# Optimization experiments

Measured on AMD Instinct MI355X. Metric: run time of the kernel, lower is better.

The kernel has to match this reference:

```python
import jax, jax.numpy as jnp
import numpy as np

B, SQ, SK, H, NH = 4, 512, 2048, 1024, 16
HD = H // NH
LN_EPS = 1e-12
NEG_INF = float('-inf')


def setup_inputs() -> dict:
    key = jax.random.key(0)
    ks = jax.random.split(key, 6)
    hidden_states = jax.random.normal(ks[0], (B, SQ, H), dtype=jnp.float32)
    encoder_hidden_states = jax.random.normal(ks[1], (B, SK, H), dtype=jnp.float32)
    mask = jax.random.randint(ks[2], (B, SK), 0, 2).astype(jnp.int32)
    mask = mask.at[:, 0].set(1)  # guarantee >=1 valid key per row (avoid all -inf softmax)
    scale = 1.0 / np.sqrt(H)
    q_w = jax.random.normal(ks[3], (H, H), dtype=jnp.float32) * scale
    k_w = jax.random.normal(ks[4], (H, H), dtype=jnp.float32) * scale
    return {
        'hidden_states': hidden_states,
        'encoder_hidden_states': encoder_hidden_states,
        'encoder_attention_mask': mask,
        'q_w': q_w,
        'q_b': jnp.zeros((H,), jnp.float32),
        'k_w': k_w,
        'k_b': jnp.zeros((H,), jnp.float32),
        'ln_g': jnp.ones((H,), jnp.float32),
        'ln_b': jnp.zeros((H,), jnp.float32),
    }


def _layernorm(x, g, b):
    mu = jnp.mean(x, axis=-1, keepdims=True)
    var = jnp.mean(jnp.square(x - mu), axis=-1, keepdims=True)
    return (x - mu) * jax.lax.rsqrt(var + LN_EPS) * g + b


def reference(hidden_states, encoder_hidden_states, encoder_attention_mask,
              q_w, q_b, k_w, k_b, ln_g, ln_b):
    bsz, sq, _ = hidden_states.shape
    hs = _layernorm(hidden_states, ln_g, ln_b)
    # torch Linear: y = x @ W.T + b
    q = (hs @ q_w.T + q_b).reshape(bsz, sq, NH, HD).transpose(0, 2, 1, 3)      # b h q d
    k = (encoder_hidden_states @ k_w.T + k_b).reshape(bsz, -1, NH, HD).transpose(0, 2, 1, 3)  # b h k d
    v = encoder_hidden_states.reshape(bsz, -1, NH, HD).transpose(0, 2, 1, 3)   # b h k d (no v projection)
    scores = jnp.einsum('bhqd,bhkd->bhqk', q, k) / np.sqrt(HD)
    scores = jnp.where(encoder_attention_mask[:, None, None, :] == 0, NEG_INF, scores)
    probs = jax.nn.softmax(scores, axis=-1)
    ctx = jnp.einsum('bhqk,bhkd->bhqd', probs, v)
    ctx = ctx.transpose(0, 2, 1, 3).reshape(bsz, sq, H)
    return ctx, scores
```

## Files before the change

kernel.cpp:

```cpp
#include <hip/hip_runtime.h>
#include <math.h>

#define H 1024
#define NH 16
#define HD 64
#define B_ 4
#define SQ 512
#define SK 2048
#define MASKED_SCORE -1e30f

typedef unsigned short ushort_t;
typedef __attribute__((ext_vector_type(8))) short short8_t;
typedef __attribute__((ext_vector_type(4))) float f32x4;
typedef __attribute__((ext_vector_type(4))) unsigned short us4;

__device__ inline ushort_t bf_hi(float x) { return (ushort_t)(__float_as_uint(x) >> 16); }
__device__ inline ushort_t bf_lo(float x) {
    float hf = __uint_as_float(__float_as_uint(x) & 0xffff0000u);
    return (ushort_t)(__float_as_uint(x - hf) >> 16);
}

__global__ __launch_bounds__(256) void ln_split_kernel(const float* __restrict__ x,
                                                       const float* __restrict__ g,
                                                       const float* __restrict__ bb,
                                                       ushort_t* __restrict__ hi,
                                                       ushort_t* __restrict__ lo) {
    const int row = blockIdx.x;
    const int tid = threadIdx.x;
    const float4 v = *(const float4*)&x[(size_t)row * H + tid * 4];
    float s  = v.x + v.y + v.z + v.w;
    float ss = v.x * v.x + v.y * v.y + v.z * v.z + v.w * v.w;
    #pragma unroll
    for (int o = 32; o > 0; o >>= 1) { s += __shfl_down(s, o); ss += __shfl_down(ss, o); }
    __shared__ float red_s[4], red_ss[4];
    const int wv = tid >> 6, ln = tid & 63;
    if (ln == 0) { red_s[wv] = s; red_ss[wv] = ss; }
    __syncthreads();
    s  = red_s[0] + red_s[1] + red_s[2] + red_s[3];
    ss = red_ss[0] + red_ss[1] + red_ss[2] + red_ss[3];
    const float mu   = s * (1.0f / H);
    const float var  = ss * (1.0f / H) - mu * mu;
    const float rstd = rsqrtf(var + 1e-12f);
    const float4 gv = *(const float4*)&g[tid * 4];
    const float4 bv = *(const float4*)&bb[tid * 4];
    float o0 = (v.x - mu) * rstd * gv.x + bv.x;
    float o1 = (v.y - mu) * rstd * gv.y + bv.y;
    float o2 = (v.z - mu) * rstd * gv.z + bv.z;
    float o3 = (v.w - mu) * rstd * gv.w + bv.w;
    us4 h4, l4;
    h4.x = bf_hi(o0); h4.y = bf_hi(o1); h4.z = bf_hi(o2); h4.w = bf_hi(o3);
    l4.x = bf_lo(o0); l4.y = bf_lo(o1); l4.z = bf_lo(o2); l4.w = bf_lo(o3);
    *(us4*)&hi[(size_t)row * H + tid * 4] = h4;
    *(us4*)&lo[(size_t)row * H + tid * 4] = l4;
}

__global__ __launch_bounds__(256) void ehs_split_tr(const float* __restrict__ ehs,
                                                    ushort_t* __restrict__ eh, ushort_t* __restrict__ el,
                                                    ushort_t* __restrict__ vh, ushort_t* __restrict__ vl) {
    __shared__ float Tf[64][68];
    const int tid = threadIdx.x;
    const int k0 = blockIdx.x * 64;
    const int h = blockIdx.y, b = blockIdx.z;
    const int r = tid >> 2, c0 = (tid & 3) << 4;
    const size_t gidx = (size_t)(b * SK + k0 + r) * H + h * HD + c0;
    float fv[16];
    #pragma unroll
    for (int j = 0; j < 4; ++j) {
        const float4 v = *(const float4*)&ehs[gidx + 4 * j];
        fv[4 * j + 0] = v.x; fv[4 * j + 1] = v.y; fv[4 * j + 2] = v.z; fv[4 * j + 3] = v.w;
        Tf[r][c0 + 4 * j + 0] = v.x; Tf[r][c0 + 4 * j + 1] = v.y;
        Tf[r][c0 + 4 * j + 2] = v.z; Tf[r][c0 + 4 * j + 3] = v.w;
    }
    short8_t H0, H1, L0, L1;
    #pragma unroll
    for (int j = 0; j < 8; ++j) {
        H0[j] = (short)bf_hi(fv[j]);     H1[j] = (short)bf_hi(fv[8 + j]);
        L0[j] = (short)bf_lo(fv[j]);     L1[j] = (short)bf_lo(fv[8 + j]);
    }
    *(short8_t*)&eh[gidx] = H0; *(short8_t*)&eh[gidx + 8] = H1;
    *(short8_t*)&el[gidx] = L0; *(short8_t*)&el[gidx + 8] = L1;
    __syncthreads();
    const int d = tid >> 2, kb = (tid & 3) << 4;
    float tv[16];
    #pragma unroll
    for (int i = 0; i < 16; ++i) tv[i] = Tf[kb + i][d];
    short8_t Vh0, Vh1, Vl0, Vl1;
    #pragma unroll
    for (int j = 0; j < 8; ++j) {
        Vh0[j] = (short)bf_hi(tv[j]);     Vh1[j] = (short)bf_hi(tv[8 + j]);
        Vl0[j] = (short)bf_lo(tv[j]);     Vl1[j] = (short)bf_lo(tv[8 + j]);
    }
    const size_t vg = ((size_t)((b * NH + h) * HD + d)) * SK + k0 + kb;
    *(short8_t*)&vh[vg] = Vh0; *(short8_t*)&vh[vg + 8] = Vh1;
    *(short8_t*)&vl[vg] = Vl0; *(short8_t*)&vl[vg + 8] = Vl1;
}

__global__ __launch_bounds__(256) void split2_kernel(const float* __restrict__ s0,
                                                     const float* __restrict__ s1,
                                                     ushort_t* __restrict__ h0, ushort_t* __restrict__ l0,
                                                     ushort_t* __restrict__ h1, ushort_t* __restrict__ l1,
                                                     int n4) {
    int i = blockIdx.x * 256 + threadIdx.x;
    const float* src; ushort_t* hi; ushort_t* lo;
    if (i < n4) { src = s0; hi = h0; lo = l0; }
    else        { src = s1; hi = h1; lo = l1; i -= n4; }
    const float4 v = ((const float4*)src)[i];
    us4 h4, l4;
    h4.x = bf_hi(v.x); h4.y = bf_hi(v.y); h4.z = bf_hi(v.z); h4.w = bf_hi(v.w);
    l4.x = bf_lo(v.x); l4.y = bf_lo(v.y); l4.z = bf_lo(v.z); l4.w = bf_lo(v.w);
    ((us4*)hi)[i] = h4;
    ((us4*)lo)[i] = l4;
}

__global__ __launch_bounds__(256, 2) void gemm_dual(
        const ushort_t* __restrict__ QAh, const ushort_t* __restrict__ QAl,
        const ushort_t* __restrict__ QWh_g, const ushort_t* __restrict__ QWl_g,
        const float* __restrict__ q_bias, ushort_t* __restrict__ QCh, ushort_t* __restrict__ QCl,
        const ushort_t* __restrict__ KAh, const ushort_t* __restrict__ KAl,
        const ushort_t* __restrict__ KWh_g, const ushort_t* __restrict__ KWl_g,
        const float* __restrict__ k_bias, ushort_t* __restrict__ KCh, ushort_t* __restrict__ KCl) {
    __shared__ ushort_t Ah[128 * 64], Al[128 * 64], Wh[128 * 64], Wl[128 * 64];
    const int tid = threadIdx.x;
    const int cpx = gridDim.x >> 3;
    const int L = ((int)blockIdx.x & 7) * cpx + ((int)blockIdx.x >> 3);
    const bool isQ = L < 128;
    const int Li = isQ ? L : L - 128;
    const ushort_t* Ah_g = isQ ? QAh : KAh;
    const ushort_t* Al_g = isQ ? QAl : KAl;
    const ushort_t* Wh_g = isQ ? QWh_g : KWh_g;
    const ushort_t* Wl_g = isQ ? QWl_g : KWl_g;
    const float*    bias = isQ ? q_bias : k_bias;
    ushort_t* Chi = isQ ? QCh : KCh;
    ushort_t* Clo = isQ ? QCl : KCl;
    const int m0 = (Li >> 3) * 128, n0 = (Li & 7) * 128;
    const int lane = tid & 63, wid = tid >> 6;
    const int wr = wid >> 1, wc = wid & 1;
    const int fr = lane & 15, fs = lane >> 4;

    int srow[4], sch[4], lidx[4];
    #pragma unroll
    for (int i = 0; i < 4; ++i) {
        const int c = i * 256 + tid;
        srow[i] = c >> 3; sch[i] = c & 7;
        lidx[i] = srow[i] * 64 + ((sch[i] ^ (srow[i] & 7)) << 3);
    }

    short8_t rAh[4], rAl[4], rWh[4], rWl[4];
    auto gload = [&](int k0) {
        #pragma unroll
        for (int i = 0; i < 4; ++i) {
            const size_t ga = (size_t)(m0 + srow[i]) * H + k0 + (sch[i] << 3);
            const size_t gw = (size_t)(n0 + srow[i]) * H + k0 + (sch[i] << 3);
            rAh[i] = *(const short8_t*)&Ah_g[ga];
            rAl[i] = *(const short8_t*)&Al_g[ga];
            rWh[i] = *(const short8_t*)&Wh_g[gw];
            rWl[i] = *(const short8_t*)&Wl_g[gw];
        }
    };

    f32x4 acc[4][4];
    #pragma unroll
    for (int i = 0; i < 4; ++i)
        #pragma unroll
        for (int j = 0; j < 4; ++j) acc[i][j] = (f32x4)0.f;

    gload(0);
    for (int kt = 0; kt < 16; ++kt) {
        #pragma unroll
        for (int i = 0; i < 4; ++i) {
            *(short8_t*)&Ah[lidx[i]] = rAh[i];
            *(short8_t*)&Al[lidx[i]] = rAl[i];
            *(short8_t*)&Wh[lidx[i]] = rWh[i];
            *(short8_t*)&Wl[lidx[i]] = rWl[i];
        }
        __syncthreads();
        if (kt < 15) gload((kt + 1) * 64);
        #pragma unroll
        for (int ks = 0; ks < 2; ++ks) {
            short8_t ah[4], al[4], bh[4], bl[4];
            #pragma unroll
            for (int mi = 0; mi < 4; ++mi) {
                const int rr = wr * 64 + mi * 16 + fr;
                const int idx = rr * 64 + ((((ks << 2) + fs) ^ (rr & 7)) << 3);
                ah[mi] = *(const short8_t*)&Ah[idx];
                al[mi] = *(const short8_t*)&Al[idx];
            }
            #pragma unroll
            for (int ni = 0; ni < 4; ++ni) {
                const int rr = wc * 64 + ni * 16 + fr;
                const int idx = rr * 64 + ((((ks << 2) + fs) ^ (rr & 7)) << 3);
                bh[ni] = *(const short8_t*)&Wh[idx];
                bl[ni] = *(const short8_t*)&Wl[idx];
            }
            #pragma unroll
            for (int mi = 0; mi < 4; ++mi)
                #pragma unroll
                for (int ni = 0; ni < 4; ++ni) {
                    acc[mi][ni] = __builtin_amdgcn_mfma_f32_16x16x32_bf16(ah[mi], bh[ni], acc[mi][ni], 0, 0, 0);
                    acc[mi][ni] = __builtin_amdgcn_mfma_f32_16x16x32_bf16(ah[mi], bl[ni], acc[mi][ni], 0, 0, 0);
                    acc[mi][ni] = __builtin_amdgcn_mfma_f32_16x16x32_bf16(al[mi], bh[ni], acc[mi][ni], 0, 0, 0);
                }
        }
        __syncthreads();
    }
    #pragma unroll
    for (int ni = 0; ni < 4; ++ni) {
        const int col = n0 + wc * 64 + ni * 16 + fr;
        const float bv = bias[col];
        #pragma unroll
        for (int mi = 0; mi < 4; ++mi) {
            const int row = m0 + wr * 64 + mi * 16 + (fs << 2);
            #pragma unroll
            for (int r2 = 0; r2 < 4; ++r2) {
                const float v = acc[mi][ni][r2] + bv;
                Chi[(size_t)(row + r2) * H + col] = bf_hi(v);
                Clo[(size_t)(row + r2) * H + col] = bf_lo(v);
            }
        }
    }
}

#define SIDX(q, c) ((q) * 64 + ((((c)) ^ ((q) & 15)) << 2))
__global__ __launch_bounds__(256, 2) void attn_mfma(
        const ushort_t* __restrict__ Qh_g, const ushort_t* __restrict__ Ql_g,
        const ushort_t* __restrict__ Kh_g, const ushort_t* __restrict__ Kl_g,
        const ushort_t* __restrict__ Vh_g, const ushort_t* __restrict__ Vl_g,
        const int* __restrict__ mask,
        float* __restrict__ ctx_out, float* __restrict__ sc_out) {
    __shared__ ushort_t QS[2 * 64 * 64];
    __shared__ ushort_t Kh[64 * 64], Kl[64 * 64];
    __shared__ ushort_t Vh[64 * 64], Vl[64 * 64];
    __shared__ ushort_t Ph[64 * 72], Pl[64 * 72];
    __shared__ int Ms[64];
    float* Sbuf = (float*)QS;
    const int tid = threadIdx.x, lane = tid & 63, w = tid >> 6;
    const int fr = lane & 15, fs = lane >> 4;
    const int L = ((int)blockIdx.x & 7) * 64 + ((int)blockIdx.x >> 3);
    const int b = L >> 7, h = (L >> 3) & 15, q0 = (L & 7) * 64;

    int srow[2], sch[2], lidx[2];
    #pragma unroll
    for (int i = 0; i < 2; ++i) {
        const int c = i * 256 + tid;
        srow[i] = c >> 3; sch[i] = c & 7;
        lidx[i] = srow[i] * 64 + ((sch[i] ^ (srow[i] & 7)) << 3);
    }

    short8_t rk[8];
    auto kvload = [&](int k0) {
        #pragma unroll
        for (int i = 0; i < 2; ++i) {
            const size_t gk = (size_t)(b * SK + k0 + srow[i]) * H + h * HD + (sch[i] << 3);
            const size_t gv = ((size_t)((b * NH + h) * HD + srow[i])) * SK + k0 + (sch[i] << 3);
            rk[0 + i] = *(const short8_t*)&Kh_g[gk];
            rk[2 + i] = *(const short8_t*)&Kl_g[gk];
            rk[4 + i] = *(const short8_t*)&Vh_g[gv];
            rk[6 + i] = *(const short8_t*)&Vl_g[gv];
        }
    };
    auto kvwrite = [&]() {
        #pragma unroll
        for (int i = 0; i < 2; ++i) {
            *(short8_t*)&Kh[lidx[i]] = rk[0 + i];
            *(short8_t*)&Kl[lidx[i]] = rk[2 + i];
            *(short8_t*)&Vh[lidx[i]] = rk[4 + i];
            *(short8_t*)&Vl[lidx[i]] = rk[6 + i];
        }
    };

    {
        short8_t rq[4];
        #pragma unroll
        for (int i = 0; i < 2; ++i) {
            const size_t gq = (size_t)(b * SQ + q0 + srow[i]) * H + h * HD + (sch[i] << 3);
            rq[i]     = *(const short8_t*)&Qh_g[gq];
            rq[2 + i] = *(const short8_t*)&Ql_g[gq];
        }
        kvload(0);
        #pragma unroll
        for (int i = 0; i < 2; ++i) {
            *(short8_t*)&QS[lidx[i]]        = rq[i];
            *(short8_t*)&QS[4096 + lidx[i]] = rq[2 + i];
        }
        kvwrite();
        if (tid < 64) Ms[tid] = mask[b * SK + tid];
    }
    __syncthreads();

    short8_t qh[2], ql[2];
    #pragma unroll
    for (int ks = 0; ks < 2; ++ks) {
        const int rr = w * 16 + fr;
        const int idx = rr * 64 + ((((ks << 2) + fs) ^ (rr & 7)) << 3);
        qh[ks] = *(const short8_t*)&QS[idx];
        ql[ks] = *(const short8_t*)&QS[4096 + idx];
    }
    __syncthreads();

    f32x4 cacc[4];
    #pragma unroll
    for (int ni = 0; ni < 4; ++ni) cacc[ni] = (f32x4)0.f;
    float m_r[4] = {-INFINITY, -INFINITY, -INFINITY, -INFINITY};
    float l_r[4] = {0.f, 0.f, 0.f, 0.f};

    const int oq = tid >> 2, oc0 = (tid & 3) << 2;
    const size_t sobase = ((size_t)((b * NH + h) * SQ + q0 + oq)) * SK;

    int mreg = 0;
    for (int kc = 0; kc < 32; ++kc) {
        const int k0 = kc * 64;
        if (kc < 31) {
            kvload(k0 + 64);
            if (tid < 64) mreg = mask[b * SK + k0 + 64 + tid];
        }
        f32x4 sacc[4];
        #pragma unroll
        for (int ni = 0; ni < 4; ++ni) sacc[ni] = (f32x4)0.f;
        #pragma unroll
        for (int ks = 0; ks < 2; ++ks) {
            short8_t kbh[4], kbl[4];
            #pragma unroll
            for (int ni = 0; ni < 4; ++ni) {
                const int rr = ni * 16 + fr;
                const int idx = rr * 64 + ((((ks << 2) + fs) ^ (rr & 7)) << 3);
                kbh[ni] = *(const short8_t*)&Kh[idx];
                kbl[ni] = *(const short8_t*)&Kl[idx];
            }
            #pragma unroll
            for (int ni = 0; ni < 4; ++ni) {
                sacc[ni] = __builtin_amdgcn_mfma_f32_16x16x32_bf16(qh[ks], kbh[ni], sacc[ni], 0, 0, 0);
                sacc[ni] = __builtin_amdgcn_mfma_f32_16x16x32_bf16(qh[ks], kbl[ni], sacc[ni], 0, 0, 0);
                sacc[ni] = __builtin_amdgcn_mfma_f32_16x16x32_bf16(ql[ks], kbh[ni], sacc[ni], 0, 0, 0);
            }
        }
        int mv[4];
        #pragma unroll
        for (int ni = 0; ni < 4; ++ni) mv[ni] = Ms[ni * 16 + fr];

        #pragma unroll
        for (int r2 = 0; r2 < 4; ++r2) {
            const int q = w * 16 + (fs << 2) + r2;
            float sv[4];
            #pragma unroll
            for (int ni = 0; ni < 4; ++ni) sv[ni] = sacc[ni][r2] * 0.125f;
            #pragma unroll
            for (int ni = 0; ni < 4; ++ni) {
                const int c = (ni << 2) + (fr >> 2);
                Sbuf[SIDX(q, c) + (fr & 3)] = mv[ni] ? sv[ni] : MASKED_SCORE;
            }
            float x0 = mv[0] ? sv[0] : -INFINITY;
            float x1 = mv[1] ? sv[1] : -INFINITY;
            float x2 = mv[2] ? sv[2] : -INFINITY;
            float x3 = mv[3] ? sv[3] : -INFINITY;
            float cm = fmaxf(fmaxf(x0, x1), fmaxf(x2, x3));
            cm = fmaxf(cm, __shfl_xor(cm, 1));
            cm = fmaxf(cm, __shfl_xor(cm, 2));
            cm = fmaxf(cm, __shfl_xor(cm, 4));
            cm = fmaxf(cm, __shfl_xor(cm, 8));
            if (cm > m_r[r2]) {
                const float mn = cm;
                const float scf = (m_r[r2] == -INFINITY) ? 0.f : __expf(m_r[r2] - mn);
                l_r[r2] *= scf;
                #pragma unroll
                for (int ni = 0; ni < 4; ++ni) cacc[ni][r2] *= scf;
                m_r[r2] = mn;
            }
            float p[4], ps = 0.f;
            #pragma unroll
            for (int ni = 0; ni < 4; ++ni) {
                p[ni] = mv[ni] ? __expf(sv[ni] - m_r[r2]) : 0.f;
                ps += p[ni];
            }
            ps += __shfl_xor(ps, 1);
            ps += __shfl_xor(ps, 2);
            ps += __shfl_xor(ps, 4);
            ps += __shfl_xor(ps, 8);
            l_r[r2] += ps;
            #pragma unroll
            for (int ni = 0; ni < 4; ++ni) {
                Ph[q * 72 + ni * 16 + fr] = bf_hi(p[ni]);
                Pl[q * 72 + ni * 16 + fr] = bf_lo(p[ni]);
            }
        }
        #pragma unroll
        for (int ks = 0; ks < 2; ++ks) {
            const int pidx = (w * 16 + fr) * 72 + ks * 32 + (fs << 3);
            const short8_t pah = *(const short8_t*)&Ph[pidx];
            const short8_t pal = *(const short8_t*)&Pl[pidx];
            #pragma unroll
            for (int ni = 0; ni < 4; ++ni) {
                const int rr = ni * 16 + fr;
                const int idx = rr * 64 + ((((ks << 2) + fs) ^ (rr & 7)) << 3);
                const short8_t vbh = *(const short8_t*)&Vh[idx];
                const short8_t vbl = *(const short8_t*)&Vl[idx];
                cacc[ni] = __builtin_amdgcn_mfma_f32_16x16x32_bf16(pah, vbh, cacc[ni], 0, 0, 0);
                cacc[ni] = __builtin_amdgcn_mfma_f32_16x16x32_bf16(pah, vbl, cacc[ni], 0, 0, 0);
                cacc[ni] = __builtin_amdgcn_mfma_f32_16x16x32_bf16(pal, vbh, cacc[ni], 0, 0, 0);
            }
        }
        __syncthreads();
        #pragma unroll
        for (int j = 0; j < 4; ++j) {
            const int c = oc0 + j;
            const float4 v4 = *(const float4*)&Sbuf[SIDX(oq, c)];
            *(float4*)&sc_out[sobase + k0 + (c << 2)] = v4;
        }
        if (kc < 31) {
            kvwrite();
            if (tid < 64) Ms[tid] = mreg;
        }
        __syncthreads();
    }
    #pragma unroll
    for (int ni = 0; ni < 4; ++ni)
        #pragma unroll
        for (int r2 = 0; r2 < 4; ++r2) {
            const float v = cacc[ni][r2] / l_r[r2];
            ctx_out[(size_t)(b * SQ + q0 + w * 16 + (fs << 2) + r2) * H + h * HD + ni * 16 + fr] = v;
        }
}

extern "C" void kernel_launch(void* const* d_in, const int* in_sizes, int n_in,
                              void* d_out, int out_size, void* d_ws, size_t ws_size,
                              hipStream_t stream) {
    const float* hs_in = (const float*)d_in[0];
    const float* ehs   = (const float*)d_in[1];
    const int*   msk   = (const int*)d_in[2];
    const float* q_w   = (const float*)d_in[3];
    const float* q_b   = (const float*)d_in[4];
    const float* k_w   = (const float*)d_in[5];
    const float* k_b   = (const float*)d_in[6];
    const float* ln_g  = (const float*)d_in[7];
    const float* ln_b  = (const float*)d_in[8];

    float* ctx = (float*)d_out;
    float* sc  = ctx + (size_t)B_ * SQ * H;

    ushort_t* wsu = (ushort_t*)d_ws;
    ushort_t* Vth = wsu;
    ushort_t* Vtl = Vth + (size_t)8 * 1024 * 1024;
    ushort_t* Khp = Vtl + (size_t)8 * 1024 * 1024;
    ushort_t* Klp = Khp + (size_t)8 * 1024 * 1024;
    ushort_t* Qhp = Klp + (size_t)8 * 1024 * 1024;
    ushort_t* Qlp = Qhp + (size_t)2 * 1024 * 1024;

    ushort_t* scr = (ushort_t*)sc;
    ushort_t* Ehp = scr;
    ushort_t* Elp = Ehp + (size_t)8 * 1024 * 1024;
    ushort_t* HSh = Elp + (size_t)8 * 1024 * 1024;
    ushort_t* HSl = HSh + (size_t)2 * 1024 * 1024;
    ushort_t* QWh = HSl + (size_t)2 * 1024 * 1024;
    ushort_t* QWl = QWh + (size_t)1024 * 1024;
    ushort_t* KWh = QWl + (size_t)1024 * 1024;
    ushort_t* KWl = KWh + (size_t)1024 * 1024;

    ln_split_kernel<<<B_ * SQ, 256, 0, stream>>>(hs_in, ln_g, ln_b, HSh, HSl);
    ehs_split_tr<<<dim3(SK / 64, NH, B_), 256, 0, stream>>>(ehs, Ehp, Elp, Vth, Vtl);
    split2_kernel<<<2048, 256, 0, stream>>>(q_w, k_w, QWh, QWl, KWh, KWl, (H * H) / 4);
    gemm_dual<<<640, 256, 0, stream>>>(HSh, HSl, QWh, QWl, q_b, Qhp, Qlp,
                                       Ehp, Elp, KWh, KWl, k_b, Khp, Klp);
    attn_mfma<<<512, 256, 0, stream>>>(Qhp, Qlp, Khp, Klp, Vth, Vtl, msk, ctx, sc);
}
```

Baseline: 510.5 us.

## Fuse prep kernels and transpose QK MFMA so softmax reductions stay in-lane

Merges the layernorm split, encoder-state split/transpose and weight-split kernels into one launch with block-range dispatch, removing two kernel launches. In the attention kernel, the QK^T MFMA operands are swapped so each lane holds one query row across keys. The row max and sum then need two cross-lane shuffles instead of four per row, and the per-r2 loop goes away. The mask is read straight from global memory as int4 instead of being staged in shared memory, and P is written as packed bf16 pairs into a swizzled buffer. The cost is extra shuffles to broadcast the rescale factors and more complex indexing, with some risk around the P and score layouts.

Measured after the change: 512.3 us. About the same (+0.4%).

```diff
diff --git a/kernel.cpp b/kernel.cpp
--- a/kernel.cpp
+++ b/kernel.cpp
@@ -19,97 +19,103 @@
     float hf = __uint_as_float(__float_as_uint(x) & 0xffff0000u);
     return (ushort_t)(__float_as_uint(x - hf) >> 16);
 }
-
-__global__ __launch_bounds__(256) void ln_split_kernel(const float* __restrict__ x,
-                                                       const float* __restrict__ g,
-                                                       const float* __restrict__ bb,
-                                                       ushort_t* __restrict__ hi,
-                                                       ushort_t* __restrict__ lo) {
-    const int row = blockIdx.x;
+__device__ inline unsigned pack_hi2(float a, float b) {
+    return (__float_as_uint(a) >> 16) | (__float_as_uint(b) & 0xffff0000u);
+}
+__device__ inline unsigned pack_lo2(float a, float b) {
+    const float ah = __uint_as_float(__float_as_uint(a) & 0xffff0000u);
+    const float bh = __uint_as_float(__float_as_uint(b) & 0xffff0000u);
+    const float al = a - ah, bl = b - bh;
+    return (__float_as_uint(al) >> 16) | (__float_as_uint(bl) & 0xffff0000u);
+}
+
+__global__ __launch_bounds__(256) void prep_kernel(
+        const float* __restrict__ hs, const float* __restrict__ g, const float* __restrict__ bb,
+        ushort_t* __restrict__ HSh, ushort_t* __restrict__ HSl,
+        const float* __restrict__ ehs,
+        ushort_t* __restrict__ Ehp, ushort_t* __restrict__ Elp,
+        ushort_t* __restrict__ Vth, ushort_t* __restrict__ Vtl,
+        const float* __restrict__ qw, const float* __restrict__ kw,
+        ushort_t* __restrict__ QWh, ushort_t* __restrict__ QWl,
+        ushort_t* __restrict__ KWh, ushort_t* __restrict__ KWl) {
+    __shared__ float Tf[64][68];
+    __shared__ float red_s[4], red_ss[4];
     const int tid = threadIdx.x;
-    const float4 v = *(const float4*)&x[(size_t)row * H + tid * 4];
-    float s  = v.x + v.y + v.z + v.w;
-    float ss = v.x * v.x + v.y * v.y + v.z * v.z + v.w * v.w;
-    #pragma unroll
-    for (int o = 32; o > 0; o >>= 1) { s += __shfl_down(s, o); ss += __shfl_down(ss, o); }
-    __shared__ float red_s[4], red_ss[4];
-    const int wv = tid >> 6, ln = tid & 63;
-    if (ln == 0) { red_s[wv] = s; red_ss[wv] = ss; }
-    __syncthreads();
-    s  = red_s[0] + red_s[1] + red_s[2] + red_s[3];
-    ss = red_ss[0] + red_ss[1] + red_ss[2] + red_ss[3];
-    const float mu   = s * (1.0f / H);
-    const float var  = ss * (1.0f / H) - mu * mu;
-    const float rstd = rsqrtf(var + 1e-12f);
-    const float4 gv = *(const float4*)&g[tid * 4];
-    const float4 bv = *(const float4*)&bb[tid * 4];
-    float o0 = (v.x - mu) * rstd * gv.x + bv.x;
-    float o1 = (v.y - mu) * rstd * gv.y + bv.y;
-    float o2 = (v.z - mu) * rstd * gv.z + bv.z;
-    float o3 = (v.w - mu) * rstd * gv.w + bv.w;
-    us4 h4, l4;
-    h4.x = bf_hi(o0); h4.y = bf_hi(o1); h4.z = bf_hi(o2); h4.w = bf_hi(o3);
-    l4.x = bf_lo(o0); l4.y = bf_lo(o1); l4.z = bf_lo(o2); l4.w = bf_lo(o3);
-    *(us4*)&hi[(size_t)row * H + tid * 4] = h4;
-    *(us4*)&lo[(size_t)row * H + tid * 4] = l4;
-}
-
-__global__ __launch_bounds__(256) void ehs_split_tr(const float* __restrict__ ehs,
-                                                    ushort_t* __restrict__ eh, ushort_t* __restrict__ el,
-                                                    ushort_t* __restrict__ vh, ushort_t* __restrict__ vl) {
-    __shared__ float Tf[64][68];
-    const int tid = threadIdx.x;
-    const int k0 = blockIdx.x * 64;
-    const int h = blockIdx.y, b = blockIdx.z;
-    const int r = tid >> 2, c0 = (tid & 3) << 4;
-    const size_t gidx = (size_t)(b * SK + k0 + r) * H + h * HD + c0;
-    float fv[16];
-    #pragma unroll
-    for (int j = 0; j < 4; ++j) {
-        const float4 v = *(const float4*)&ehs[gidx + 4 * j];
-        fv[4 * j + 0] = v.x; fv[4 * j + 1] = v.y; fv[4 * j + 2] = v.z; fv[4 * j + 3] = v.w;
-        Tf[r][c0 + 4 * j + 0] = v.x; Tf[r][c0 + 4 * j + 1] = v.y;
-        Tf[r][c0 + 4 * j + 2] = v.z; Tf[r][c0 + 4 * j + 3] = v.w;
-    }
-    short8_t H0, H1, L0, L1;
-    #pragma unroll
-    for (int j = 0; j < 8; ++j) {
-        H0[j] = (short)bf_hi(fv[j]);     H1[j] = (short)bf_hi(fv[8 + j]);
-        L0[j] = (short)bf_lo(fv[j]);     L1[j] = (short)bf_lo(fv[8 + j]);
-    }
-    *(short8_t*)&eh[gidx] = H0; *(short8_t*)&eh[gidx + 8] = H1;
-    *(short8_t*)&el[gidx] = L0; *(short8_t*)&el[gidx + 8] = L1;
-    __syncthreads();
-    const int d = tid >> 2, kb = (tid & 3) << 4;
-    float tv[16];
-    #pragma unroll
-    for (int i = 0; i < 16; ++i) tv[i] = Tf[kb + i][d];
-    short8_t Vh0, Vh1, Vl0, Vl1;
-    #pragma unroll
-    for (int j = 0; j < 8; ++j) {
-        Vh0[j] = (short)bf_hi(tv[j]);     Vh1[j] = (short)bf_hi(tv[8 + j]);
-        Vl0[j] = (short)bf_lo(tv[j]);     Vl1[j] = (short)bf_lo(tv[8 + j]);
-    }
-    const size_t vg = ((size_t)((b * NH + h) * HD + d)) * SK + k0 + kb;
-    *(short8_t*)&vh[vg] = Vh0; *(short8_t*)&vh[vg + 8] = Vh1;
-    *(short8_t*)&vl[vg] = Vl0; *(short8_t*)&vl[vg + 8] = Vl1;
-}
-
-__global__ __launch_bounds__(256) void split2_kernel(const float* __restrict__ s0,
-                                                     const float* __restrict__ s1,
-                                                     ushort_t* __restrict__ h0, ushort_t* __restrict__ l0,
-                                                     ushort_t* __restrict__ h1, ushort_t* __restrict__ l1,
-                                                     int n4) {
-    int i = blockIdx.x * 256 + threadIdx.x;
-    const float* src; ushort_t* hi; ushort_t* lo;
-    if (i < n4) { src = s0; hi = h0; lo = l0; }
-    else        { src = s1; hi = h1; lo = l1; i -= n4; }
-    const float4 v = ((const float4*)src)[i];
-    us4 h4, l4;
-    h4.x = bf_hi(v.x); h4.y = bf_hi(v.y); h4.z = bf_hi(v.z); h4.w = bf_hi(v.w);
-    l4.x = bf_lo(v.x); l4.y = bf_lo(v.y); l4.z = bf_lo(v.z); l4.w = bf_lo(v.w);
-    ((us4*)hi)[i] = h4;
-    ((us4*)lo)[i] = l4;
+    const int bid = blockIdx.x;
+    if (bid < 2048) {
+        const int row = bid;
+        const float4 v = *(const float4*)&hs[(size_t)row * H + tid * 4];
+        float s  = v.x + v.y + v.z + v.w;
+        float ss = v.x * v.x + v.y * v.y + v.z * v.z + v.w * v.w;
+        #pragma unroll
+        for (int o = 32; o > 0; o >>= 1) { s += __shfl_down(s, o); ss += __shfl_down(ss, o); }
+        const int wv = tid >> 6, lnn = tid & 63;
+        if (lnn == 0) { red_s[wv] = s; red_ss[wv] = ss; }
+        __syncthreads();
+        s  = red_s[0] + red_s[1] + red_s[2] + red_s[3];
+        ss = red_ss[0] + red_ss[1] + red_ss[2] + red_ss[3];
+        const float mu   = s * (1.0f / H);
+        const float var  = ss * (1.0f / H) - mu * mu;
+        const float rstd = rsqrtf(var + 1e-12f);
+        const float4 gv = *(const float4*)&g[tid * 4];
+        const float4 bv = *(const float4*)&bb[tid * 4];
+        const float o0 = (v.x - mu) * rstd * gv.x + bv.x;
+        const float o1 = (v.y - mu) * rstd * gv.y + bv.y;
+        const float o2 = (v.z - mu) * rstd * gv.z + bv.z;
+        const float o3 = (v.w - mu) * rstd * gv.w + bv.w;
+        us4 h4, l4;
+        h4.x = bf_hi(o0); h4.y = bf_hi(o1); h4.z = bf_hi(o2); h4.w = bf_hi(o3);
+        l4.x = bf_lo(o0); l4.y = bf_lo(o1); l4.z = bf_lo(o2); l4.w = bf_lo(o3);
+        *(us4*)&HSh[(size_t)row * H + tid * 4] = h4;
+        *(us4*)&HSl[(size_t)row * H + tid * 4] = l4;
+    } else if (bid < 4096) {
+        const int id = bid - 2048;
+        const int k0 = (id & 31) * 64, h = (id >> 5) & 15, b = id >> 9;
+        const int r = tid >> 2, c0 = (tid & 3) << 4;
+        const size_t gidx = (size_t)(b * SK + k0 + r) * H + h * HD + c0;
+        float fv[16];
+        #pragma unroll
+        for (int j = 0; j < 4; ++j) {
+            const float4 v = *(const float4*)&ehs[gidx + 4 * j];
+            fv[4 * j + 0] = v.x; fv[4 * j + 1] = v.y; fv[4 * j + 2] = v.z; fv[4 * j + 3] = v.w;
+            Tf[r][c0 + 4 * j + 0] = v.x; Tf[r][c0 + 4 * j + 1] = v.y;
+            Tf[r][c0 + 4 * j + 2] = v.z; Tf[r][c0 + 4 * j + 3] = v.w;
+        }
+        short8_t H0, H1, L0, L1;
+        #pragma unroll
+        for (int j = 0; j < 8; ++j) {
+            H0[j] = (short)bf_hi(fv[j]);     H1[j] = (short)bf_hi(fv[8 + j]);
+            L0[j] = (short)bf_lo(fv[j]);     L1[j] = (short)bf_lo(fv[8 + j]);
+        }
+        *(short8_t*)&Ehp[gidx] = H0; *(short8_t*)&Ehp[gidx + 8] = H1;
+        *(short8_t*)&Elp[gidx] = L0; *(short8_t*)&Elp[gidx + 8] = L1;
+        __syncthreads();
+        const int d = tid >> 2, kb = (tid & 3) << 4;
+        float tv[16];
+        #pragma unroll
+        for (int i = 0; i < 16; ++i) tv[i] = Tf[kb + i][d];
+        short8_t Vh0, Vh1, Vl0, Vl1;
+        #pragma unroll
+        for (int j = 0; j < 8; ++j) {
+            Vh0[j] = (short)bf_hi(tv[j]);     Vh1[j] = (short)bf_hi(tv[8 + j]);
+            Vl0[j] = (short)bf_lo(tv[j]);     Vl1[j] = (short)bf_lo(tv[8 + j]);
+        }
+        const size_t vg = ((size_t)((b * NH + h) * HD + d)) * SK + k0 + kb;
+        *(short8_t*)&Vth[vg] = Vh0; *(short8_t*)&Vth[vg + 8] = Vh1;
+        *(short8_t*)&Vtl[vg] = Vl0; *(short8_t*)&Vtl[vg + 8] = Vl1;
+    } else {
+        int i = (bid - 4096) * 256 + tid;
+        const int half = (H * H) / 4;
+        const float* src; ushort_t* hi; ushort_t* lo;
+        if (i < half) { src = qw; hi = QWh; lo = QWl; }
+        else          { src = kw; hi = KWh; lo = KWl; i -= half; }
+        const float4 v = ((const float4*)src)[i];
+        us4 h4, l4;
+        h4.x = bf_hi(v.x); h4.y = bf_hi(v.y); h4.z = bf_hi(v.z); h4.w = bf_hi(v.w);
+        l4.x = bf_lo(v.x); l4.y = bf_lo(v.y); l4.z = bf_lo(v.z); l4.w = bf_lo(v.w);
+        ((us4*)hi)[i] = h4;
+        ((us4*)lo)[i] = l4;
+    }
 }
 
 __global__ __launch_bounds__(256, 2) void gemm_dual(
@@ -230,8 +236,7 @@
     __shared__ ushort_t QS[2 * 64 * 64];
     __shared__ ushort_t Kh[64 * 64], Kl[64 * 64];
     __shared__ ushort_t Vh[64 * 64], Vl[64 * 64];
-    __shared__ ushort_t Ph[64 * 72], Pl[64 * 72];
-    __shared__ int Ms[64];
+    __shared__ unsigned Pws[2][2048];
     float* Sbuf = (float*)QS;
     const int tid = threadIdx.x, lane = tid & 63, w = tid >> 6;
     const int fr = lane & 15, fs = lane >> 4;
@@ -283,7 +288,6 @@
             *(short8_t*)&QS[4096 + lidx[i]] = rq[2 + i];
         }
         kvwrite();
-        if (tid < 64) Ms[tid] = mask[b * SK + tid];
     }
     __syncthreads();
 
@@ -300,19 +304,21 @@
     f32x4 cacc[4];
     #pragma unroll
     for (int ni = 0; ni < 4; ++ni) cacc[ni] = (f32x4)0.f;
-    float m_r[4] = {-INFINITY, -INFINITY, -INFINITY, -INFINITY};
-    float l_r[4] = {0.f, 0.f, 0.f, 0.f};
+    float m_r = -INFINITY, l_r = 0.f;
 
     const int oq = tid >> 2, oc0 = (tid & 3) << 2;
     const size_t sobase = ((size_t)((b * NH + h) * SQ + q0 + oq)) * SK;
-
-    int mreg = 0;
+    const int Sq = w * 16 + fr;
+    const int pwbase = (w << 9) + (fr << 5);
+
     for (int kc = 0; kc < 32; ++kc) {
         const int k0 = kc * 64;
-        if (kc < 31) {
-            kvload(k0 + 64);
-            if (tid < 64) mreg = mask[b * SK + k0 + 64 + tid];
-        }
+        if (kc < 31) kvload(k0 + 64);
+        int4 mv4[4];
+        #pragma unroll
+        for (int ni = 0; ni < 4; ++ni)
+            mv4[ni] = *(const int4*)&mask[b * SK + k0 + (ni << 4) + (fs << 2)];
+
         f32x4 sacc[4];
         #pragma unroll
         for (int ni = 0; ni < 4; ++ni) sacc[ni] = (f32x4)0.f;
@@ -321,75 +327,87 @@
             short8_t kbh[4], kbl[4];
             #pragma unroll
             for (int ni = 0; ni < 4; ++ni) {
-                const int rr = ni * 16 + fr;
+                const int rr = (ni << 4) + fr;
                 const int idx = rr * 64 + ((((ks << 2) + fs) ^ (rr & 7)) << 3);
                 kbh[ni] = *(const short8_t*)&Kh[idx];
                 kbl[ni] = *(const short8_t*)&Kl[idx];
             }
             #pragma unroll
             for (int ni = 0; ni < 4; ++ni) {
-                sacc[ni] = __builtin_amdgcn_mfma_f32_16x16x32_bf16(qh[ks], kbh[ni], sacc[ni], 0, 0, 0);
-                sacc[ni] = __builtin_amdgcn_mfma_f32_16x16x32_bf16(qh[ks], kbl[ni], sacc[ni], 0, 0, 0);
-                sacc[ni] = __builtin_amdgcn_mfma_f32_16x16x32_bf16(ql[ks], kbh[ni], sacc[ni], 0, 0, 0);
-            }
-        }
-        int mv[4];
-        #pragma unroll
-        for (int ni = 0; ni < 4; ++ni) mv[ni] = Ms[ni * 16 + fr];
-
-        #pragma unroll
-        for (int r2 = 0; r2 < 4; ++r2) {
-            const int q = w * 16 + (fs << 2) + r2;
-            float sv[4];
-            #pragma unroll
-            for (int ni = 0; ni < 4; ++ni) sv[ni] = sacc[ni][r2] * 0.125f;
+                sacc[ni] = __builtin_amdgcn_mfma_f32_16x16x32_bf16(kbh[ni], qh[ks], sacc[ni], 0, 0, 0);
+                sacc[ni] = __builtin_amdgcn_mfma_f32_16x16x32_bf16(kbh[ni], ql[ks], sacc[ni], 0, 0, 0);
+                sacc[ni] = __builtin_amdgcn_mfma_f32_16x16x32_bf16(kbl[ni], qh[ks], sacc[ni], 0, 0, 0);
+            }
+        }
+
+        float p[4][4];
+        float cm = -INFINITY;
+        #pragma unroll
+        for (int ni = 0; ni < 4; ++ni) {
+            const int mk[4] = {mv4[ni].x, mv4[ni].y, mv4[ni].z, mv4[ni].w};
+            float4 o;
+            float x[4];
+            #pragma unroll
+            for (int r2 = 0; r2 < 4; ++r2) {
+                const float sv = sacc[ni][r2] * 0.125f;
+                x[r2] = mk[r2] ? sv : -INFINITY;
+            }
+            o.x = mk[0] ? x[0] : MASKED_SCORE;
+            o.y = mk[1] ? x[1] : MASKED_SCORE;
+            o.z = mk[2] ? x[2] : MASKED_SCORE;
+            o.w = mk[3] ? x[3] : MASKED_SCORE;
+            *(float4*)&Sbuf[SIDX(Sq, (ni << 2) + fs)] = o;
+            p[ni][0] = x[0]; p[ni][1] = x[1]; p[ni][2] = x[2]; p[ni][3] = x[3];
+            cm = fmaxf(cm, fmaxf(fmaxf(x[0], x[1]), fmaxf(x[2], x[3])));
+        }
+        cm = fmaxf(cm, __shfl_xor(cm, 16));
+        cm = fmaxf(cm, __shfl_xor(cm, 32));
+        float scf = 1.f;
+        if (cm > m_r) {
+            scf = (m_r == -INFINITY) ? 0.f : __expf(m_r - cm);
+            m_r = cm;
+        }
+        l_r *= scf;
+        float ps = 0.f;
+        #pragma unroll
+        for (int ni = 0; ni < 4; ++ni)
+            #pragma unroll
+            for (int r2 = 0; r2 < 4; ++r2) {
+                const float e = (p[ni][r2] == -INFINITY) ? 0.f : __expf(p[ni][r2] - m_r);
+                p[ni][r2] = e;
+                ps += e;
+            }
+        ps += __shfl_xor(ps, 16);
+        ps += __shfl_xor(ps, 32);
+        l_r += ps;
+        float scf4[4];
+        #pragma unroll
+        for (int r2 = 0; r2 < 4; ++r2) scf4[r2] = __shfl(scf, (fs << 2) + r2);
+        #pragma unroll
+        for (int ni = 0; ni < 4; ++ni)
+            #pragma unroll
+            for (int r2 = 0; r2 < 4; ++r2) cacc[ni][r2] *= scf4[r2];
+        #pragma unroll
+        for (int ni = 0; ni < 4; ++ni) {
+            uint2 hv, lv;
+            hv.x = pack_hi2(p[ni][0], p[ni][1]);
+            hv.y = pack_hi2(p[ni][2], p[ni][3]);
+            lv.x = pack_lo2(p[ni][0], p[ni][1]);
+            lv.y = pack_lo2(p[ni][2], p[ni][3]);
+            const int pidx = pwbase + ((ni ^ (fr & 3)) << 3) + (fs << 1);
+            *(uint2*)&Pws[0][pidx] = hv;
+            *(uint2*)&Pws[1][pidx] = lv;
+        }
+
+        #pragma unroll
+        for (int ks = 0; ks < 2; ++ks) {
+            const int ni_src = (ks << 1) + (fs >> 1);
+            const int pr = pwbase + ((ni_src ^ (fr & 3)) << 3) + ((fs & 1) << 2);
+            const short8_t pah = *(const short8_t*)&Pws[0][pr];
+            const short8_t pal = *(const short8_t*)&Pws[1][pr];
             #pragma unroll
             for (int ni = 0; ni < 4; ++ni) {
-                const int c = (ni << 2) + (fr >> 2);
-                Sbuf[SIDX(q, c) + (fr & 3)] = mv[ni] ? sv[ni] : MASKED_SCORE;
-            }
-            float x0 = mv[0] ? sv[0] : -INFINITY;
-            float x1 = mv[1] ? sv[1] : -INFINITY;
-            float x2 = mv[2] ? sv[2] : -INFINITY;
-            float x3 = mv[3] ? sv[3] : -INFINITY;
-            float cm = fmaxf(fmaxf(x0, x1), fmaxf(x2, x3));
-            cm = fmaxf(cm, __shfl_xor(cm, 1));
-            cm = fmaxf(cm, __shfl_xor(cm, 2));
-            cm = fmaxf(cm, __shfl_xor(cm, 4));
-            cm = fmaxf(cm, __shfl_xor(cm, 8));
-            if (cm > m_r[r2]) {
-                const float mn = cm;
-                const float scf = (m_r[r2] == -INFINITY) ? 0.f : __expf(m_r[r2] - mn);
-                l_r[r2] *= scf;
-                #pragma unroll
-                for (int ni = 0; ni < 4; ++ni) cacc[ni][r2] *= scf;
-                m_r[r2] = mn;
-            }
-            float p[4], ps = 0.f;
-            #pragma unroll
-            for (int ni = 0; ni < 4; ++ni) {
-                p[ni] = mv[ni] ? __expf(sv[ni] - m_r[r2]) : 0.f;
-                ps += p[ni];
-            }
-            ps += __shfl_xor(ps, 1);
-            ps += __shfl_xor(ps, 2);
-            ps += __shfl_xor(ps, 4);
-            ps += __shfl_xor(ps, 8);
-            l_r[r2] += ps;
-            #pragma unroll
-            for (int ni = 0; ni < 4; ++ni) {
-                Ph[q * 72 + ni * 16 + fr] = bf_hi(p[ni]);
-                Pl[q * 72 + ni * 16 + fr] = bf_lo(p[ni]);
-            }
-        }
-        #pragma unroll
-        for (int ks = 0; ks < 2; ++ks) {
-            const int pidx = (w * 16 + fr) * 72 + ks * 32 + (fs << 3);
-            const short8_t pah = *(const short8_t*)&Ph[pidx];
-            const short8_t pal = *(const short8_t*)&Pl[pidx];
-            #pragma unroll
-            for (int ni = 0; ni < 4; ++ni) {
-                const int rr = ni * 16 + fr;
+                const int rr = (ni << 4) + fr;
                 const int idx = rr * 64 + ((((ks << 2) + fs) ^ (rr & 7)) << 3);
                 const short8_t vbh = *(const short8_t*)&Vh[idx];
                 const short8_t vbl = *(const short8_t*)&Vl[idx];
@@ -405,19 +423,18 @@
             const float4 v4 = *(const float4*)&Sbuf[SIDX(oq, c)];
             *(float4*)&sc_out[sobase + k0 + (c << 2)] = v4;
         }
-        if (kc < 31) {
-            kvwrite();
-            if (tid < 64) Ms[tid] = mreg;
-        }
-        __syncthreads();
-    }
+        if (kc < 31) kvwrite();
+        __syncthreads();
+    }
+    float linv[4];
+    #pragma unroll
+    for (int r2 = 0; r2 < 4; ++r2) linv[r2] = 1.0f / __shfl(l_r, (fs << 2) + r2);
     #pragma unroll
     for (int ni = 0; ni < 4; ++ni)
         #pragma unroll
-        for (int r2 = 0; r2 < 4; ++r2) {
-            const float v = cacc[ni][r2] / l_r[r2];
-            ctx_out[(size_t)(b * SQ + q0 + w * 16 + (fs << 2) + r2) * H + h * HD + ni * 16 + fr] = v;
-        }
+        for (int r2 = 0; r2 < 4; ++r2)
+            ctx_out[(size_t)(b * SQ + q0 + w * 16 + (fs << 2) + r2) * H + h * HD + (ni << 4) + fr] =
+                cacc[ni][r2] * linv[r2];
 }
 
 extern "C" void kernel_launch(void* const* d_in, const int* in_sizes, int n_in,
@@ -454,9 +471,9 @@
     ushort_t* KWh = QWl + (size_t)1024 * 1024;
     ushort_t* KWl = KWh + (size_t)1024 * 1024;
 
-    ln_split_kernel<<<B_ * SQ, 256, 0, stream>>>(hs_in, ln_g, ln_b, HSh, HSl);
-    ehs_split_tr<<<dim3(SK / 64, NH, B_), 256, 0, stream>>>(ehs, Ehp, Elp, Vth, Vtl);
-    split2_kernel<<<2048, 256, 0, stream>>>(q_w, k_w, QWh, QWl, KWh, KWl, (H * H) / 4);
+    prep_kernel<<<6144, 256, 0, stream>>>(hs_in, ln_g, ln_b, HSh, HSl,
+                                          ehs, Ehp, Elp, Vth, Vtl,
+                                          q_w, k_w, QWh, QWl, KWh, KWl);
     gemm_dual<<<640, 256, 0, stream>>>(HSh, HSl, QWh, QWl, q_b, Qhp, Qlp,
                                        Ehp, Elp, KWh, KWl, k_b, Khp, Klp);
     attn_mfma<<<512, 256, 0, stream>>>(Qhp, Qlp, Khp, Klp, Vth, Vtl, msk, ctx, sc);
```
